# Optimization experiments

Hardware: AMD Instinct MI355X
Metric: run time of the kernel (lower is better)

The kernel has to match this reference:

```python
import jax, jax.numpy as jnp
import numpy as np
import math

DIM = 2048
N_HEADS = 32
N_KV_HEADS = 8
HEAD_DIM = DIM // N_HEADS  # 64
N_REP = N_HEADS // N_KV_HEADS  # 4
BATCH = 1
SEQ = 2048


def rope_cos_sin(seq_len, head_dim, dtype=jnp.float32):
    inv_freq = 1.0 / (10000.0 ** (jnp.arange(0, head_dim, 2, dtype=jnp.float32) / head_dim))
    t = jnp.arange(seq_len, dtype=jnp.float32)
    freqs = jnp.outer(t, inv_freq)            # [S, D/2]
    emb = jnp.concatenate([freqs, freqs], -1)  # [S, D]
    return jnp.cos(emb).astype(dtype), jnp.sin(emb).astype(dtype)


def rotate_half(x):
    x1 = x[..., ::2]
    x2 = x[..., 1::2]
    return jnp.concatenate([-x2, x1], axis=-1)


def setup_inputs() -> dict:
    key = jax.random.key(0)
    ks = jax.random.split(key, 5)
    scale = 1.0 / math.sqrt(DIM)
    x = jax.random.normal(ks[0], (BATCH, SEQ, DIM), jnp.float32)
    wq = jax.random.normal(ks[1], (DIM, N_HEADS * HEAD_DIM), jnp.float32) * scale
    wk = jax.random.normal(ks[2], (DIM, N_KV_HEADS * HEAD_DIM), jnp.float32) * scale
    wv = jax.random.normal(ks[3], (DIM, N_KV_HEADS * HEAD_DIM), jnp.float32) * scale
    wo = jax.random.normal(ks[4], (N_HEADS * HEAD_DIM, DIM), jnp.float32) * scale
    mask = jnp.tril(jnp.ones((SEQ, SEQ), jnp.int32))[None, None]  # [1,1,S,S]
    return {"x": x, "mask": mask, "wq": wq, "wk": wk, "wv": wv, "wo": wo}


def reference(x, mask, wq, wk, wv, wo):
    B, S, _ = x.shape
    q = (x @ wq).reshape(B, S, N_HEADS, HEAD_DIM).transpose(0, 2, 1, 3)     # [B,H,S,D]
    k = (x @ wk).reshape(B, S, N_KV_HEADS, HEAD_DIM).transpose(0, 2, 1, 3)  # [B,Hkv,S,D]
    v = (x @ wv).reshape(B, S, N_KV_HEADS, HEAD_DIM).transpose(0, 2, 1, 3)
    cos, sin = rope_cos_sin(S, HEAD_DIM)  # [S,D]
    q = q * cos + rotate_half(q) * sin
    k = k * cos + rotate_half(k) * sin
    if N_REP > 1:
        k = jnp.repeat(k, N_REP, axis=1)
        v = jnp.repeat(v, N_REP, axis=1)
    scores = jnp.einsum("bhqd,bhkd->bhqk", q, k) / math.sqrt(HEAD_DIM)
    scores = jnp.where(mask == 0, -jnp.inf, scores)
    attn = jax.nn.softmax(scores, axis=-1)
    out = jnp.einsum("bhqk,bhkd->bhqd", attn, v)  # [B,H,S,D]
    out = out.transpose(0, 2, 1, 3).reshape(B, S, N_HEADS * HEAD_DIM)
    return out @ wo
```

## Files before the change

kernel.cpp:

```cpp
#include <hip/hip_runtime.h>
#include <hip/hip_bf16.h>

#define DIM 2048
#define SEQ 2048
#define NH 32
#define HD 64
#define NKV 8
#define QKV_LD 3072

typedef __attribute__((ext_vector_type(8))) short bf16x8;
typedef __attribute__((ext_vector_type(4))) float f32x4;
typedef __attribute__((ext_vector_type(2))) unsigned int uint2v;
typedef unsigned short ushort_t;

__device__ inline unsigned short f2bf(float f) {
    union { float f; unsigned int u; } v; v.f = f;
    unsigned int r = v.u + 0x7fffu + ((v.u >> 16) & 1u);
    return (unsigned short)(r >> 16);
}
__device__ inline float bf2f(ushort_t u) {
    union { unsigned int u; float f; } v; v.u = ((unsigned int)u) << 16; return v.f;
}

__device__ inline void async_cp16(const void* g, void* l) {
    __builtin_amdgcn_global_load_lds(
        (const __attribute__((address_space(1))) unsigned int*)g,
        (__attribute__((address_space(3))) unsigned int*)l, 16, 0, 0);
}

__device__ inline void pswap32(unsigned int& a, unsigned int& b) {
    uint2v r = __builtin_amdgcn_permlane32_swap(a, b, false, false);
    a = r[0]; b = r[1];
}
__device__ inline void pswap16(unsigned int& a, unsigned int& b) {
    uint2v r = __builtin_amdgcn_permlane16_swap(a, b, false, false);
    a = r[0]; b = r[1];
}
__device__ inline float wave_max(float x) {
    unsigned int a = __float_as_uint(x), b = a;
    uint2v r = __builtin_amdgcn_permlane16_swap(a, b, false, false);
    x = fmaxf(__uint_as_float(r[0]), __uint_as_float(r[1]));
    a = __float_as_uint(x); b = a;
    r = __builtin_amdgcn_permlane32_swap(a, b, false, false);
    return fmaxf(__uint_as_float(r[0]), __uint_as_float(r[1]));
}
__device__ inline float wave_sum(float x) {
    unsigned int a = __float_as_uint(x), b = a;
    uint2v r = __builtin_amdgcn_permlane16_swap(a, b, false, false);
    x = __uint_as_float(r[0]) + __uint_as_float(r[1]);
    a = __float_as_uint(x); b = a;
    r = __builtin_amdgcn_permlane32_swap(a, b, false, false);
    return __uint_as_float(r[0]) + __uint_as_float(r[1]);
}
__device__ inline unsigned int cvt_pk_bf16(float lo, float hi) {
    unsigned int r;
    asm volatile("v_cvt_pk_bf16_f32 %0, %1, %2" : "=v"(r) : "v"(lo), "v"(hi));
    return r;
}

__global__ __launch_bounds__(256) void convert_kernel(
    const float* __restrict__ X, ushort_t* __restrict__ Xb)
{
    int i = (blockIdx.x * 256 + threadIdx.x) * 4;
    float4 v = *(const float4*)(X + i);
    ushort_t o[4] = { f2bf(v.x), f2bf(v.y), f2bf(v.z), f2bf(v.w) };
    *(uint2*)(Xb + i) = *(uint2*)o;
}

__global__ __launch_bounds__(256) void transpose_kernel(
    const float* __restrict__ W, ushort_t* __restrict__ WT, int N)
{
    __shared__ __align__(16) ushort_t tile[64][72];
    const int n0 = blockIdx.x * 64, k0 = blockIdx.y * 64;
    const int t = threadIdx.x;
    {
        const int tk = t >> 4;
        const int tn = (t & 15) * 4;
        #pragma unroll
        for (int i = 0; i < 4; i++) {
            const int k = tk + i * 16;
            float4 v = *(const float4*)(W + (size_t)(k0 + k) * N + n0 + tn);
            tile[tn + 0][k] = f2bf(v.x);
            tile[tn + 1][k] = f2bf(v.y);
            tile[tn + 2][k] = f2bf(v.z);
            tile[tn + 3][k] = f2bf(v.w);
        }
    }
    __syncthreads();
    {
        const int tn = t >> 2;
        const int tk = (t & 3) * 16;
        uint4 a = *(const uint4*)&tile[tn][tk];
        uint4 b = *(const uint4*)&tile[tn][tk + 8];
        ushort_t* dst = WT + (size_t)(n0 + tn) * DIM + k0 + tk;
        *(uint4*)dst = a;
        *(uint4*)(dst + 8) = b;
    }
}

template<int OUT_F32>
__global__ __launch_bounds__(256) void gemm_kernel(
    const ushort_t* __restrict__ A, const ushort_t* __restrict__ BT,
    void* __restrict__ Cout, int K, int lda, int ldo)
{
    __shared__ __align__(16) ushort_t sA[128 * 32];
    __shared__ __align__(16) ushort_t sB[128 * 32];
    const int tn = blockIdx.x * 128, tm = blockIdx.y * 128;
    const int t = threadIdx.x, wave = t >> 6, lane = t & 63;
    const int m16 = lane & 15, quad = lane >> 4;
    const int wr = (wave >> 1) * 64, wc = (wave & 1) * 64;
    const int srow = lane >> 2;
    const int sce = (lane & 3) * 8;

    f32x4 acc[4][4] = {};

    for (int k0 = 0; k0 < K; k0 += 32) {
        __syncthreads();
        #pragma unroll
        for (int p = 0; p < 2; p++) {
            const int j = wave * 2 + p;
            const int row = j * 16 + srow;
            async_cp16(A  + (size_t)(tm + row) * lda + k0 + sce, &sA[j * 512]);
            async_cp16(BT + (size_t)(tn + row) * K   + k0 + sce, &sB[j * 512]);
        }
        __syncthreads();
        bf16x8 af[4], bf[4];
        #pragma unroll
        for (int mt = 0; mt < 4; mt++)
            af[mt] = *(const bf16x8*)&sA[(wr + mt * 16 + m16) * 32 + quad * 8];
        #pragma unroll
        for (int nt = 0; nt < 4; nt++)
            bf[nt] = *(const bf16x8*)&sB[(wc + nt * 16 + m16) * 32 + quad * 8];
        #pragma unroll
        for (int mt = 0; mt < 4; mt++)
            #pragma unroll
            for (int nt = 0; nt < 4; nt++)
                acc[mt][nt] = __builtin_amdgcn_mfma_f32_16x16x32_bf16(af[mt], bf[nt], acc[mt][nt], 0, 0, 0);
    }

    #pragma unroll
    for (int mt = 0; mt < 4; mt++) {
        const int row = tm + wr + mt * 16 + quad * 4;
        #pragma unroll
        for (int nt = 0; nt < 4; nt++) {
            const int col = tn + wc + nt * 16 + m16;
            #pragma unroll
            for (int r = 0; r < 4; r++) {
                if (OUT_F32)
                    ((float*)Cout)[(size_t)(row + r) * ldo + col] = acc[mt][nt][r];
                else
                    ((ushort_t*)Cout)[(size_t)(row + r) * ldo + col] = f2bf(acc[mt][nt][r]);
            }
        }
    }
}

#define QSCALE 0.18033688011112042f
__global__ __launch_bounds__(256) void rope_kernel(ushort_t* qkv, ushort_t* __restrict__ Kr)
{
    const int gid = blockIdx.x * 256 + threadIdx.x;
    const int lane = gid & 63;
    const int idx = gid >> 6;
    const int s = idx / 40;
    const int hh = idx - s * 40;

    const ushort_t* src;
    ushort_t* dst;
    const bool isq = (hh < 32);
    if (isq) {
        dst = qkv + (size_t)s * QKV_LD + hh * 64;
        src = dst;
    } else {
        src = qkv + (size_t)s * QKV_LD + 2048 + (hh - 32) * 64;
        dst = Kr + ((size_t)(hh - 32) * SEQ + s) * 64;
    }

    const float e = bf2f(src[lane]);
    const int i = lane & 31;
    const float freq = __expf(-(float)i * 0.28782313662425572f);
    const float ang = (float)s * freq;
    const float cv = cosf(ang), sv = sinf(ang);
    const int partner = (lane < 32) ? (2 * lane + 1) : (2 * (lane - 32));
    const float y = __shfl(e, partner, 64);
    float out = (lane < 32) ? (e * cv - y * sv) : (e * cv + y * sv);
    if (isq) out *= QSCALE;
    dst[lane] = f2bf(out);
}

__global__ __launch_bounds__(256) void vtrans_kernel(
    const ushort_t* __restrict__ qkv, ushort_t* __restrict__ Vt)
{
    __shared__ __align__(16) ushort_t tile[64][72];
    const int kvh = blockIdx.x & 7;
    const int s0 = (blockIdx.x >> 3) * 64;
    const int t = threadIdx.x;
    {
        const int sr = t >> 3;
        const int d8 = (t & 7) * 8;
        #pragma unroll
        for (int i = 0; i < 2; i++) {
            const int s = sr + i * 32;
            ushort_t tmp[8];
            *(uint4*)tmp = *(const uint4*)(qkv + (size_t)(s0 + s) * QKV_LD + 2560 + kvh * 64 + d8);
            #pragma unroll
            for (int j = 0; j < 8; j++) tile[d8 + j][s] = tmp[j];
        }
    }
    __syncthreads();
    {
        const int dr = t >> 3;
        const int s8 = (t & 7) * 8;
        #pragma unroll
        for (int i = 0; i < 2; i++) {
            const int d = dr + i * 32;
            *(uint4*)(Vt + ((size_t)kvh * 64 + d) * SEQ + s0 + s8) = *(const uint4*)&tile[d][s8];
        }
    }
}

#define MFMA16(A, B, C) __builtin_amdgcn_mfma_f32_16x16x32_bf16(A, B, C, 0, 0, 0)

#define LOADK(KF, KB) do { \
    _Pragma("unroll") \
    for (int _k = 0; _k < 4; _k++) { \
        const ushort_t* _kp = Krh + (size_t)((KB) + _k * 16 + m16) * 64 + quad * 8; \
        KF[_k][0] = *(const bf16x8*)_kp; \
        KF[_k][1] = *(const bf16x8*)(_kp + 32); \
    } \
} while (0)

#define LOADV(VF, KB) do { \
    _Pragma("unroll") \
    for (int _n = 0; _n < 4; _n++) { \
        const ushort_t* _vp = Vth + (size_t)(_n * 16 + m16) * SEQ + (KB) + quad * 8; \
        VF[_n][0] = *(const bf16x8*)_vp; \
        VF[_n][1] = *(const bf16x8*)(_vp + 32); \
    } \
} while (0)

#define QKT(SC, KF, QA) do { \
    _Pragma("unroll") \
    for (int _k = 0; _k < 4; _k++) { \
        SC[_k] = MFMA16(KF[_k][0], qf[QA][0], SC[_k]); \
        SC[_k] = MFMA16(KF[_k][1], qf[QA][1], SC[_k]); \
    } \
} while (0)

#define SMPV(SC, QA, DOMASK, KBASE, VF) do { \
    float s_[16]; \
    _Pragma("unroll") \
    for (int _k = 0; _k < 4; _k++) { \
        _Pragma("unroll") \
        for (int _r = 0; _r < 4; _r++) { \
            float _v = SC[_k][_r]; \
            if ((DOMASK) && ((KBASE) + _k * 16 + quad * 4 + _r > qi[QA])) _v = -1e30f; \
            s_[_k * 4 + _r] = _v; \
        } \
    } \
    float _x0 = fmaxf(s_[0], s_[1]),   _x1 = fmaxf(s_[2], s_[3]); \
    float _x2 = fmaxf(s_[4], s_[5]),   _x3 = fmaxf(s_[6], s_[7]); \
    float _x4 = fmaxf(s_[8], s_[9]),   _x5 = fmaxf(s_[10], s_[11]); \
    float _x6 = fmaxf(s_[12], s_[13]), _x7 = fmaxf(s_[14], s_[15]); \
    float _rmax = fmaxf(fmaxf(fmaxf(_x0, _x1), fmaxf(_x2, _x3)), \
                        fmaxf(fmaxf(_x4, _x5), fmaxf(_x6, _x7))); \
    _rmax = wave_max(_rmax); \
    if (_rmax > m_run[QA] + 8.f) { \
        const float _mnew = fmaxf(m_run[QA], _rmax); \
        const float _alpha = __builtin_amdgcn_exp2f(m_run[QA] - _mnew); \
        m_run[QA] = _mnew; \
        l_run[QA] *= _alpha; \
        _Pragma("unroll") \
        for (int _n = 0; _n < 4; _n++) { \
            _Pragma("unroll") \
            for (int _r = 0; _r < 4; _r++) oacc[QA][_n][_r] *= _alpha; \
        } \
    } \
    const float _m = m_run[QA]; \
    _Pragma("unroll") \
    for (int _i = 0; _i < 16; _i++) s_[_i] = __builtin_amdgcn_exp2f(s_[_i] - _m); \
    float _y0 = s_[0] + s_[1],   _y1 = s_[2] + s_[3]; \
    float _y2 = s_[4] + s_[5],   _y3 = s_[6] + s_[7]; \
    float _y4 = s_[8] + s_[9],   _y5 = s_[10] + s_[11]; \
    float _y6 = s_[12] + s_[13], _y7 = s_[14] + s_[15]; \
    float _ps = ((_y0 + _y1) + (_y2 + _y3)) + ((_y4 + _y5) + (_y6 + _y7)); \
    l_run[QA] += wave_sum(_ps); \
    unsigned int _u00 = cvt_pk_bf16(s_[0],  s_[1]),  _u01 = cvt_pk_bf16(s_[2],  s_[3]); \
    unsigned int _u10 = cvt_pk_bf16(s_[4],  s_[5]),  _u11 = cvt_pk_bf16(s_[6],  s_[7]); \
    unsigned int _u20 = cvt_pk_bf16(s_[8],  s_[9]),  _u21 = cvt_pk_bf16(s_[10], s_[11]); \
    unsigned int _u30 = cvt_pk_bf16(s_[12], s_[13]), _u31 = cvt_pk_bf16(s_[14], s_[15]); \
    pswap32(_u00, _u10); pswap16(_u00, _u10); \
    pswap32(_u01, _u11); pswap16(_u01, _u11); \
    pswap32(_u20, _u30); pswap16(_u20, _u30); \
    pswap32(_u21, _u31); pswap16(_u21, _u31); \
    union { unsigned int w[4]; bf16x8 v; } _P0, _P1; \
    _P0.w[0] = _u00; _P0.w[1] = _u01; _P0.w[2] = _u10; _P0.w[3] = _u11; \
    _P1.w[0] = _u20; _P1.w[1] = _u21; _P1.w[2] = _u30; _P1.w[3] = _u31; \
    __builtin_amdgcn_s_setprio(1); \
    _Pragma("unroll") \
    for (int _n = 0; _n < 4; _n++) { \
        oacc[QA][_n] = MFMA16(VF[_n][0], _P0.v, oacc[QA][_n]); \
        oacc[QA][_n] = MFMA16(VF[_n][1], _P1.v, oacc[QA][_n]); \
    } \
    __builtin_amdgcn_s_setprio(0); \
} while (0)

__global__ __launch_bounds__(512, 2) void attn_kernel(
    ushort_t* qkv, const ushort_t* __restrict__ Kr, const ushort_t* __restrict__ Vt)
{
    const int t = threadIdx.x, wave = t >> 6, lane = t & 63;
    const int m16 = lane & 15, quad = lane >> 4;
    const int b = blockIdx.x;
    const int kvh = b & 7;
    const int h = kvh * 4 + ((b >> 3) & 3);
    const int p = b >> 5;
    const int grp = wave >> 2;
    const int w4 = wave & 3;
    const int band = grp ? p : 15 - p;

    const ushort_t* Krh = Kr + (size_t)kvh * SEQ * 64;
    const ushort_t* Vth = Vt + (size_t)kvh * 64 * SEQ;

    const int nkt = band * 2 + 2;

    int qi[2];
    bf16x8 qf[2][2];
    #pragma unroll
    for (int qa = 0; qa < 2; qa++) {
        qi[qa] = band * 128 + (w4 + qa * 4) * 16 + m16;
        const ushort_t* qp = qkv + (size_t)qi[qa] * QKV_LD + h * 64 + quad * 8;
        qf[qa][0] = *(const bf16x8*)qp;
        qf[qa][1] = *(const bf16x8*)(qp + 32);
    }

    f32x4 oacc[2][4] = {};
    float m_run[2] = { -1e30f, -1e30f };
    float l_run[2] = { 0.f, 0.f };

    bf16x8 kfA[4][2], kfB[4][2], vf[4][2];
    LOADK(kfA, 0);

    for (int kt = 0; kt < nkt; kt += 2) {
        const bool lastpair = (kt == nkt - 2);
        const int kb0 = kt * 64, kb1 = kb0 + 64;

        f32x4 scA0[4] = {}, scA1[4] = {};
        __builtin_amdgcn_s_setprio(1);
        QKT(scA0, kfA, 0);
        QKT(scA1, kfA, 1);
        __builtin_amdgcn_s_setprio(0);
        LOADV(vf, kb0);
        LOADK(kfB, kb1);
        SMPV(scA0, 0, lastpair, kb0, vf);
        SMPV(scA1, 1, false,    kb0, vf);

        if (!lastpair) {
            f32x4 scB0[4] = {}, scB1[4] = {};
            __builtin_amdgcn_s_setprio(1);
            QKT(scB0, kfB, 0);
            QKT(scB1, kfB, 1);
            __builtin_amdgcn_s_setprio(0);
            LOADV(vf, kb1);
            LOADK(kfA, kb1 + 64);
            SMPV(scB0, 0, false, kb1, vf);
            SMPV(scB1, 1, false, kb1, vf);
        } else {
            f32x4 scB1[4] = {};
            __builtin_amdgcn_s_setprio(1);
            QKT(scB1, kfB, 1);
            __builtin_amdgcn_s_setprio(0);
            LOADV(vf, kb1);
            SMPV(scB1, 1, true, kb1, vf);
        }
    }

    #pragma unroll
    for (int qa = 0; qa < 2; qa++) {
        const float rl = 1.f / l_run[qa];
        #pragma unroll
        for (int nt = 0; nt < 4; nt++) {
            ushort_t pk[4];
            #pragma unroll
            for (int r = 0; r < 4; r++) pk[r] = f2bf(oacc[qa][nt][r] * rl);
            *(uint2*)&qkv[(size_t)qi[qa] * QKV_LD + h * 64 + nt * 16 + quad * 4] = *(uint2*)pk;
        }
    }
}

extern "C" void kernel_launch(void* const* d_in, const int* in_sizes, int n_in,
                              void* d_out, int out_size, void* d_ws, size_t ws_size,
                              hipStream_t stream)
{
    const float* x  = (const float*)d_in[0];
    const float* wq = (const float*)d_in[2];
    const float* wk = (const float*)d_in[3];
    const float* wv = (const float*)d_in[4];
    const float* wo = (const float*)d_in[5];

    ushort_t* WT  = (ushort_t*)d_ws;
    ushort_t* xb  = WT + (size_t)3072 * 2048;
    ushort_t* woT = xb;
    ushort_t* qkv = xb + (size_t)2048 * 2048;
    ushort_t* Kr  = qkv + (size_t)SEQ * QKV_LD;
    ushort_t* Vt  = Kr + (size_t)NKV * SEQ * HD;

    dim3 blk(256);

    convert_kernel<<<(DIM * SEQ) / 1024, blk, 0, stream>>>(x, xb);
    transpose_kernel<<<dim3(32, 32), blk, 0, stream>>>(wq, WT, 2048);
    transpose_kernel<<<dim3(8, 32),  blk, 0, stream>>>(wk, WT + (size_t)2048 * 2048, 512);
    transpose_kernel<<<dim3(8, 32),  blk, 0, stream>>>(wv, WT + (size_t)2560 * 2048, 512);

    gemm_kernel<0><<<dim3(QKV_LD / 128, SEQ / 128), blk, 0, stream>>>(xb, WT, qkv, DIM, DIM, QKV_LD);

    transpose_kernel<<<dim3(32, 32), blk, 0, stream>>>(wo, woT, 2048);

    rope_kernel<<<(SEQ * 40 * 64) / 256, blk, 0, stream>>>(qkv, Kr);
    vtrans_kernel<<<NKV * (SEQ / 64), blk, 0, stream>>>(qkv, Vt);

    attn_kernel<<<8 * NH, dim3(512), 0, stream>>>(qkv, Kr, Vt);

    gemm_kernel<1><<<dim3(DIM / 128, SEQ / 128), blk, 0, stream>>>(qkv, woT, d_out, DIM, QKV_LD, DIM);
}
```

Baseline: 301.8 us.

## Software-pipeline K/V global loads with inline asm and explicit vmcnt waits

Replaces the compiler-scheduled K and V fragment loads in the attention kernel with inline-asm global_load_dwordx4 pairs and manual s_waitcnt vmcnt fences. V for the next tile is now prefetched one stage earlier, overlapping with the current tile's QK^T and softmax work. The softmax and PV steps are split into separate macros so the PV MFMAs can sit after the wait. Hand-placed waitcnts and sched_barriers constrain the compiler, and the last iteration issues a dummy prefetch (kb2 = SEQ-64), which adds some wasted loads.

```diff
diff --git a/kernel.cpp b/kernel.cpp
--- a/kernel.cpp
+++ b/kernel.cpp
@@ -57,6 +57,15 @@
     asm volatile("v_cvt_pk_bf16_f32 %0, %1, %2" : "=v"(r) : "v"(lo), "v"(hi));
     return r;
 }
+
+__device__ inline void aload8(bf16x8& d0, bf16x8& d1, const ushort_t* p) {
+    asm volatile("global_load_dwordx4 %0, %2, off\n\t"
+                 "global_load_dwordx4 %1, %2, off offset:64"
+                 : "=v"(d0), "=v"(d1)
+                 : "v"(p));
+}
+#define VMWAIT8 do { asm volatile("s_waitcnt vmcnt(8)"); __builtin_amdgcn_sched_barrier(0); } while (0)
+#define VMWAIT0 do { asm volatile("s_waitcnt vmcnt(0)"); __builtin_amdgcn_sched_barrier(0); } while (0)
 
 __global__ __launch_bounds__(256) void convert_kernel(
     const float* __restrict__ X, ushort_t* __restrict__ Xb)
@@ -220,22 +229,16 @@
 
 #define MFMA16(A, B, C) __builtin_amdgcn_mfma_f32_16x16x32_bf16(A, B, C, 0, 0, 0)
 
-#define LOADK(KF, KB) do { \
-    _Pragma("unroll") \
-    for (int _k = 0; _k < 4; _k++) { \
-        const ushort_t* _kp = Krh + (size_t)((KB) + _k * 16 + m16) * 64 + quad * 8; \
-        KF[_k][0] = *(const bf16x8*)_kp; \
-        KF[_k][1] = *(const bf16x8*)(_kp + 32); \
-    } \
+#define AK(KF, KB) do { \
+    _Pragma("unroll") \
+    for (int _k = 0; _k < 4; _k++) \
+        aload8(KF[_k][0], KF[_k][1], kbp[_k] + (size_t)(KB) * 64); \
 } while (0)
 
-#define LOADV(VF, KB) do { \
-    _Pragma("unroll") \
-    for (int _n = 0; _n < 4; _n++) { \
-        const ushort_t* _vp = Vth + (size_t)(_n * 16 + m16) * SEQ + (KB) + quad * 8; \
-        VF[_n][0] = *(const bf16x8*)_vp; \
-        VF[_n][1] = *(const bf16x8*)(_vp + 32); \
-    } \
+#define AV(VF, KB) do { \
+    _Pragma("unroll") \
+    for (int _n = 0; _n < 4; _n++) \
+        aload8(VF[_n][0], VF[_n][1], vbp[_n] + (KB)); \
 } while (0)
 
 #define QKT(SC, KF, QA) do { \
@@ -246,7 +249,7 @@
     } \
 } while (0)
 
-#define SMPV(SC, QA, DOMASK, KBASE, VF) do { \
+#define SM(SC, QA, DOMASK, KBASE, OUT0, OUT1) do { \
     float s_[16]; \
     _Pragma("unroll") \
     for (int _k = 0; _k < 4; _k++) { \
@@ -295,11 +298,15 @@
     union { unsigned int w[4]; bf16x8 v; } _P0, _P1; \
     _P0.w[0] = _u00; _P0.w[1] = _u01; _P0.w[2] = _u10; _P0.w[3] = _u11; \
     _P1.w[0] = _u20; _P1.w[1] = _u21; _P1.w[2] = _u30; _P1.w[3] = _u31; \
+    OUT0 = _P0.v; OUT1 = _P1.v; \
+} while (0)
+
+#define PVX(OUT0, OUT1, VF, QA) do { \
     __builtin_amdgcn_s_setprio(1); \
     _Pragma("unroll") \
     for (int _n = 0; _n < 4; _n++) { \
-        oacc[QA][_n] = MFMA16(VF[_n][0], _P0.v, oacc[QA][_n]); \
-        oacc[QA][_n] = MFMA16(VF[_n][1], _P1.v, oacc[QA][_n]); \
+        oacc[QA][_n] = MFMA16(VF[_n][0], OUT0, oacc[QA][_n]); \
+        oacc[QA][_n] = MFMA16(VF[_n][1], OUT1, oacc[QA][_n]); \
     } \
     __builtin_amdgcn_s_setprio(0); \
 } while (0)
@@ -322,6 +329,14 @@
 
     const int nkt = band * 2 + 2;
 
+    const ushort_t* kbp[4];
+    const ushort_t* vbp[4];
+    #pragma unroll
+    for (int i = 0; i < 4; i++) {
+        kbp[i] = Krh + (size_t)(i * 16 + m16) * 64 + quad * 8;
+        vbp[i] = Vth + (size_t)(i * 16 + m16) * SEQ + quad * 8;
+    }
+
     int qi[2];
     bf16x8 qf[2][2];
     #pragma unroll
@@ -337,41 +352,50 @@
     float l_run[2] = { 0.f, 0.f };
 
     bf16x8 kfA[4][2], kfB[4][2], vf[4][2];
-    LOADK(kfA, 0);
+    AK(kfA, 0);
+    AV(vf, 0);
+    VMWAIT8;
 
     for (int kt = 0; kt < nkt; kt += 2) {
         const bool lastpair = (kt == nkt - 2);
         const int kb0 = kt * 64, kb1 = kb0 + 64;
-
-        f32x4 scA0[4] = {}, scA1[4] = {};
-        __builtin_amdgcn_s_setprio(1);
-        QKT(scA0, kfA, 0);
-        QKT(scA1, kfA, 1);
-        __builtin_amdgcn_s_setprio(0);
-        LOADV(vf, kb0);
-        LOADK(kfB, kb1);
-        SMPV(scA0, 0, lastpair, kb0, vf);
-        SMPV(scA1, 1, false,    kb0, vf);
-
-        if (!lastpair) {
-            f32x4 scB0[4] = {}, scB1[4] = {};
+        const int kb2 = lastpair ? (SEQ - 64) : (kb1 + 64);
+
+        {
+            f32x4 sc0[4] = {}, sc1[4] = {};
             __builtin_amdgcn_s_setprio(1);
-            QKT(scB0, kfB, 0);
-            QKT(scB1, kfB, 1);
+            QKT(sc0, kfA, 0);
+            QKT(sc1, kfA, 1);
             __builtin_amdgcn_s_setprio(0);
-            LOADV(vf, kb1);
-            LOADK(kfA, kb1 + 64);
-            SMPV(scB0, 0, false, kb1, vf);
-            SMPV(scB1, 1, false, kb1, vf);
-        } else {
-            f32x4 scB1[4] = {};
+            AK(kfB, kb1);
+            bf16x8 p00, p01;
+            SM(sc0, 0, lastpair, kb0, p00, p01);
+            VMWAIT8;
+            PVX(p00, p01, vf, 0);
+            bf16x8 p10, p11;
+            SM(sc1, 1, false, kb0, p10, p11);
+            PVX(p10, p11, vf, 1);
+            AV(vf, kb1);
+            VMWAIT8;
+        }
+        {
+            f32x4 sc0[4] = {}, sc1[4] = {};
             __builtin_amdgcn_s_setprio(1);
-            QKT(scB1, kfB, 1);
+            if (!lastpair) QKT(sc0, kfB, 0);
+            QKT(sc1, kfB, 1);
             __builtin_amdgcn_s_setprio(0);
-            LOADV(vf, kb1);
-            SMPV(scB1, 1, true, kb1, vf);
-        }
-    }
+            AK(kfA, kb2);
+            bf16x8 p00, p01, p10, p11;
+            if (!lastpair) SM(sc0, 0, false, kb1, p00, p01);
+            VMWAIT8;
+            if (!lastpair) PVX(p00, p01, vf, 0);
+            SM(sc1, 1, lastpair, kb1, p10, p11);
+            PVX(p10, p11, vf, 1);
+            AV(vf, kb2);
+            VMWAIT8;
+        }
+    }
+    VMWAIT0;
 
     #pragma unroll
     for (int qa = 0; qa < 2; qa++) {
```

Measured after the change: 305.6 us. Within noise of the previous version (+1.3%).
